# Kernel tuning notes

Measured on AMD Instinct MI355X. Metric: run time of the kernel, lower is better.

## Reference

```python
import jax, jax.numpy as jnp
import numpy as np

V = 32000   # vocab_size
E = 200     # embedding_size
H = 256     # LSTM hidden size (hard-coded in module)
B = 16      # batch
T = 256     # seq_len


def setup_inputs() -> dict:
    key = jax.random.key(0)
    ks = jax.random.split(key, 12)

    def init(k, shape, scale):
        return jax.random.normal(k, shape, jnp.float32) * scale

    inp = {"x": jax.random.randint(ks[0], (B, T), 0, V)}
    inp["emb"] = init(ks[1], (V, E), 0.02)
    dims = [E, H, H]
    s = 1.0 / float(np.sqrt(H))
    for l in range(3):
        inp[f"Wi{l}"] = init(ks[2 + 3 * l], (4 * H, dims[l]), s)  # input weights (gate order i,f,g,o)
        inp[f"Wh{l}"] = init(ks[3 + 3 * l], (4 * H, H), s)        # recurrent weights
        inp[f"b{l}"] = jnp.zeros((4 * H,), jnp.float32)
    inp["fcW"] = init(ks[11], (V, H), s)
    inp["fcb"] = jnp.zeros((V,), jnp.float32)
    return inp


def _lstm_layer(x, Wi, Wh, b):
    # x: [B, T, C_in] -> [B, T, H]; standard LSTM, zero initial state.
    xg = jnp.einsum('btc,gc->btg', x, Wi) + b  # precompute input projections [B,T,4H]
    Hh = Wh.shape[1]

    def step(carry, xt):
        h, c = carry
        g = xt + h @ Wh.T                      # [B, 4H]
        i, f, gg, o = jnp.split(g, 4, axis=-1)
        i = jax.nn.sigmoid(i)
        f = jax.nn.sigmoid(f)
        gg = jnp.tanh(gg)
        o = jax.nn.sigmoid(o)
        c = f * c + i * gg
        h = o * jnp.tanh(c)
        return (h, c), h

    h0 = jnp.zeros((x.shape[0], Hh), x.dtype)
    _, hs = jax.lax.scan(step, (h0, h0), jnp.swapaxes(xg, 0, 1))  # time-major scan
    return jnp.swapaxes(hs, 0, 1)


def reference(x, emb, Wi0, Wh0, b0, Wi1, Wh1, b1, Wi2, Wh2, b2, fcW, fcb):
    out = emb[x]  # [B, T, E]
    for Wi, Wh, b in ((Wi0, Wh0, b0), (Wi1, Wh1, b1), (Wi2, Wh2, b2)):
        out = _lstm_layer(out, Wi, Wh, b)
    logits = out @ fcW.T + fcb  # [B, T, V]
    return jax.nn.log_softmax(logits, axis=-1)
```

## Files before the change

kernel.cpp:

```cpp
#include <hip/hip_runtime.h>
#include <stdint.h>

typedef __attribute__((ext_vector_type(8))) short bf16x8;
typedef __attribute__((ext_vector_type(4))) float f32x4;

#define DEV __device__ __forceinline__

DEV unsigned short f2bf(float f) {
    unsigned b = __float_as_uint(f);
    unsigned r = (b + 0x7fffu + ((b >> 16) & 1u)) >> 16;
    return (unsigned short)r;
}
DEV unsigned pack2(float a, float b) {
    return (unsigned)f2bf(a) | ((unsigned)f2bf(b) << 16);
}
DEV bf16x8 pack8(float4 f0, float4 f1) {
    bf16x8 r;
    r[0] = (short)f2bf(f0.x); r[1] = (short)f2bf(f0.y);
    r[2] = (short)f2bf(f0.z); r[3] = (short)f2bf(f0.w);
    r[4] = (short)f2bf(f1.x); r[5] = (short)f2bf(f1.y);
    r[6] = (short)f2bf(f1.z); r[7] = (short)f2bf(f1.w);
    return r;
}
DEV float sigm(float x) { return 1.f / (1.f + __expf(-x)); }
DEV float tanh_f(float x) {
    float t = __expf(-2.f * fabsf(x));
    float r = (1.f - t) / (1.f + t);
    return copysignf(r, x);
}

#define OFF_HB0   65536
#define OFF_HB1   (65536 + 4194304)
#define OFF_XEA   (65536 + 8388608)
#define OFF_HS    (OFF_XEA + 2097152)

__global__ __launch_bounds__(256) void k_embed(const int* __restrict__ x,
                                               const float* __restrict__ emb,
                                               unsigned short* __restrict__ XeA)
{
    int row = blockIdx.x * 8 + (threadIdx.x >> 5);
    int i = threadIdx.x & 31;
    int tok = x[row];
    int b = row >> 8, t = row & 255;
    uint4 v = make_uint4(0, 0, 0, 0);
    if (i < 25) {
        const float* p = emb + (size_t)tok * 200 + i * 8;
        float4 f0 = *(const float4*)p;
        float4 f1 = *(const float4*)(p + 4);
        v.x = pack2(f0.x, f0.y); v.y = pack2(f0.z, f0.w);
        v.z = pack2(f1.x, f1.y); v.w = pack2(f1.z, f1.w);
    }
    int kt = i >> 2, qq = i & 3;
    *(uint4*)(XeA + (size_t)t * 4096 + (size_t)((kt * 64 + qq * 16 + b) * 8)) = v;
}

template <int OUT_F32>
__global__ __launch_bounds__(256) void k_gemm(const unsigned short* __restrict__ X, int ldx,
                                              const float* __restrict__ W, int K,
                                              const float* __restrict__ bias,
                                              unsigned short* __restrict__ outb,
                                              float* __restrict__ outf, int N)
{
    __shared__ __align__(16) unsigned short Al[128 * 72];
    __shared__ __align__(16) unsigned short Bl[128 * 72];
    const int tid = threadIdx.x, lane = tid & 63, wave = tid >> 6;
    const int wm = wave >> 1, wn = wave & 1;
    const int bm = blockIdx.y, bn = blockIdx.x;
    const int l15 = lane & 15, q = lane >> 4;

    f32x4 acc[4][4];
#pragma unroll
    for (int a = 0; a < 4; a++)
#pragma unroll
        for (int b = 0; b < 4; b++) acc[a][b] = f32x4{0.f, 0.f, 0.f, 0.f};

    for (int kb = 0; kb < 256; kb += 64) {
        __syncthreads();
#pragma unroll
        for (int it = 0; it < 4; ++it) {
            int p = tid + it * 256;
            int row = p >> 3, c8 = p & 7;
            int col = kb + c8 * 8;
            uint4 av = *(const uint4*)(X + (size_t)(bm * 128 + row) * ldx + col);
            *(uint4*)(Al + row * 72 + c8 * 8) = av;
            uint4 bv = make_uint4(0, 0, 0, 0);
            if (col < K) {
                const float* wp = W + (size_t)(bn * 128 + row) * K + col;
                float4 f0 = *(const float4*)wp;
                float4 f1 = *(const float4*)(wp + 4);
                bv.x = pack2(f0.x, f0.y); bv.y = pack2(f0.z, f0.w);
                bv.z = pack2(f1.x, f1.y); bv.w = pack2(f1.z, f1.w);
            }
            *(uint4*)(Bl + row * 72 + c8 * 8) = bv;
        }
        __syncthreads();
#pragma unroll
        for (int kt = 0; kt < 2; ++kt) {
            bf16x8 a[4], b[4];
#pragma unroll
            for (int mt = 0; mt < 4; ++mt)
                a[mt] = *(const bf16x8*)(Al + (wm * 64 + mt * 16 + l15) * 72 + kt * 32 + q * 8);
#pragma unroll
            for (int nt = 0; nt < 4; ++nt)
                b[nt] = *(const bf16x8*)(Bl + (wn * 64 + nt * 16 + l15) * 72 + kt * 32 + q * 8);
#pragma unroll
            for (int mt = 0; mt < 4; ++mt)
#pragma unroll
                for (int nt = 0; nt < 4; ++nt)
                    acc[mt][nt] = __builtin_amdgcn_mfma_f32_16x16x32_bf16(a[mt], b[nt], acc[mt][nt], 0, 0, 0);
        }
    }
#pragma unroll
    for (int nt = 0; nt < 4; ++nt) {
        int gn = bn * 128 + wn * 64 + nt * 16 + l15;
        float bv = bias[gn];
#pragma unroll
        for (int mt = 0; mt < 4; ++mt) {
#pragma unroll
            for (int r = 0; r < 4; ++r) {
                int gm = bm * 128 + wm * 64 + mt * 16 + q * 4 + r;
                float v = acc[mt][nt][r] + bv;
                if (OUT_F32) outf[(size_t)gm * N + gn] = v;
                else outb[(size_t)gm * N + gn] = f2bf(v);
            }
        }
    }
}

__global__ __launch_bounds__(256) void k_scan3(
    const float* __restrict__ Wi0, const float* __restrict__ Wh0, const float* __restrict__ b0,
    const float* __restrict__ Wi1, const float* __restrict__ Wh1, const float* __restrict__ b1,
    const float* __restrict__ Wi2, const float* __restrict__ Wh2, const float* __restrict__ b2,
    const unsigned short* __restrict__ XeA,
    unsigned short* __restrict__ hseq,
    unsigned long long* __restrict__ Hb0,
    unsigned long long* __restrict__ Hb1,
    unsigned long long* __restrict__ ring2)
{
    __shared__ __align__(16) unsigned short hX[4096];
    __shared__ __align__(16) unsigned short hH[4096];
    __shared__ float gbuf[64 * 17];
    const int tid = threadIdx.x, lane = tid & 63, wave = tid >> 6;
    const int L = blockIdx.x >> 4, s = blockIdx.x & 15;
    const int l15 = lane & 15, q = lane >> 4;
    const int grow = wave * 256 + s * 16 + l15;

    const float* Wi = (L == 0) ? Wi0 : ((L == 1) ? Wi1 : Wi2);
    const float* Wh = (L == 0) ? Wh0 : ((L == 1) ? Wh1 : Wh2);
    const float* bb = (L == 0) ? b0 : ((L == 1) ? b1 : b2);
    const int KX = (L == 0) ? 200 : 256;

    bf16x8 WiR[8], WhR[8];
#pragma unroll
    for (int kt = 0; kt < 8; ++kt) {
        int k0 = kt * 32 + q * 8;
        {
            const float* p = Wh + (size_t)grow * 256 + k0;
            WhR[kt] = pack8(*(const float4*)p, *(const float4*)(p + 4));
        }
        if (k0 < KX) {
            const float* p = Wi + (size_t)grow * KX + k0;
            WiR[kt] = pack8(*(const float4*)p, *(const float4*)(p + 4));
        } else {
            WiR[kt] = bf16x8{0, 0, 0, 0, 0, 0, 0, 0};
        }
    }
    const float bv = bb[grow];

    const int eb = tid >> 4, eu = tid & 15;
    const bool pub = (eu & 1) == 0;
    int slot;
    {
        int ug = s * 16 + eu;
        int kt = ug >> 5, qq = (ug >> 3) & 3, j = ug & 7;
        slot = ((kt * 64 + qq * 16 + eb) * 8 + j) >> 1;
    }
    float c = 0.f;
    unsigned* hX32 = (unsigned*)hX;
    unsigned* hH32 = (unsigned*)hH;

    const unsigned long long* xbase = (L == 1) ? Hb0 : Hb1;
    unsigned long long* obase = (L == 0) ? Hb0 : Hb1;
    const unsigned long long* rbase = (L == 0) ? Hb0 : Hb1;

    for (int t = 0; t < 256; ++t) {
        if (L == 0) {
            const unsigned* srcx = (const unsigned*)(XeA + (size_t)t * 4096);
            *(uint4*)(hX32 + tid * 8)     = *(const uint4*)(srcx + tid * 8);
            *(uint4*)(hX32 + tid * 8 + 4) = *(const uint4*)(srcx + tid * 8 + 4);
        }
        {
            unsigned long long vx[8], vh[8];
            unsigned pendx = (L > 0) ? 0xffu : 0u;
            unsigned pendh = (t > 0) ? 0xffu : 0u;
            const unsigned long long* sx = xbase + (size_t)t * 2048 + tid;
            const unsigned long long* sh =
                (L == 2) ? (ring2 + ((t - 1) & 1) * 2048 + tid)
                         : (rbase + (size_t)((t > 0) ? (t - 1) : 0) * 2048 + tid);
            const unsigned ex = (unsigned)(t + 1), eh = (unsigned)t;
            while (pendx | pendh) {
#pragma unroll
                for (int i = 0; i < 8; ++i)
                    if (pendx & (1u << i))
                        vx[i] = __hip_atomic_load(sx + i * 256, __ATOMIC_RELAXED,
                                                  __HIP_MEMORY_SCOPE_AGENT);
#pragma unroll
                for (int i = 0; i < 8; ++i)
                    if (pendh & (1u << i))
                        vh[i] = __hip_atomic_load(sh + i * 256, __ATOMIC_RELAXED,
                                                  __HIP_MEMORY_SCOPE_AGENT);
#pragma unroll
                for (int i = 0; i < 8; ++i) {
                    if ((pendx & (1u << i)) && (unsigned)(vx[i] >> 32) == ex) pendx &= ~(1u << i);
                    if ((pendh & (1u << i)) && (unsigned)(vh[i] >> 32) == eh) pendh &= ~(1u << i);
                }
                if (pendx | pendh) __builtin_amdgcn_s_sleep(1);
            }
            if (L > 0) {
#pragma unroll
                for (int i = 0; i < 8; ++i) hX32[tid + i * 256] = (unsigned)vx[i];
            }
            if (t > 0) {
#pragma unroll
                for (int i = 0; i < 8; ++i) hH32[tid + i * 256] = (unsigned)vh[i];
            } else {
#pragma unroll
                for (int i = 0; i < 8; ++i) hH32[tid + i * 256] = 0u;
            }
        }
        __syncthreads();

        f32x4 acc0 = {bv, bv, bv, bv};
        f32x4 acc1 = {0.f, 0.f, 0.f, 0.f};
#pragma unroll
        for (int kt = 0; kt < 8; ++kt) {
            bf16x8 ax = *(const bf16x8*)(hX + (kt * 64 + lane) * 8);
            acc0 = __builtin_amdgcn_mfma_f32_16x16x32_bf16(ax, WiR[kt], acc0, 0, 0, 0);
            bf16x8 ah = *(const bf16x8*)(hH + (kt * 64 + lane) * 8);
            acc1 = __builtin_amdgcn_mfma_f32_16x16x32_bf16(ah, WhR[kt], acc1, 0, 0, 0);
        }
        {
            int rowb = wave * 16 + l15;
#pragma unroll
            for (int r = 0; r < 4; ++r) gbuf[rowb * 17 + q * 4 + r] = acc0[r] + acc1[r];
        }
        __syncthreads();

        float gi = gbuf[(0 * 16 + eu) * 17 + eb];
        float gf = gbuf[(1 * 16 + eu) * 17 + eb];
        float gg = gbuf[(2 * 16 + eu) * 17 + eb];
        float go = gbuf[(3 * 16 + eu) * 17 + eb];
        float i_ = sigm(gi), f_ = sigm(gf), g_ = tanh_f(gg), o_ = sigm(go);
        c = f_ * c + i_ * g_;
        float h = o_ * tanh_f(c);
        float hn = __shfl_xor(h, 1);
        if (pub) {
            unsigned pk = pack2(h, hn);
            unsigned long long val =
                ((unsigned long long)(unsigned)(t + 1) << 32) | (unsigned long long)pk;
            if (L == 2) {
                __hip_atomic_store(ring2 + (t & 1) * 2048 + slot, val, __ATOMIC_RELAXED,
                                   __HIP_MEMORY_SCOPE_AGENT);
                *(unsigned*)(hseq + (size_t)(eb * 256 + t) * 256 + s * 16 + eu) = pk;
            } else {
                __hip_atomic_store(obase + (size_t)t * 2048 + slot, val, __ATOMIC_RELAXED,
                                   __HIP_MEMORY_SCOPE_AGENT);
            }
        }
    }
}

__global__ __launch_bounds__(1024) void k_lsesub(float* __restrict__ lg)
{
    __shared__ float sm[16], ss[16];
    __shared__ float sL;
    const int row = blockIdx.x, tid = threadIdx.x;
    float* p = lg + (size_t)row * 32000;
    float4 v0[4], v1[4];
    float m = -3.0e38f, s = 0.f;
#pragma unroll
    for (int k = 0; k < 4; ++k) {
        int g = tid + (k << 10);
        if (g < 4000) {
            v0[k] = *(const float4*)(p + g * 8);
            v1[k] = *(const float4*)(p + g * 8 + 4);
            float a0 = fmaxf(fmaxf(v0[k].x, v0[k].y), fmaxf(v0[k].z, v0[k].w));
            float a1 = fmaxf(fmaxf(v1[k].x, v1[k].y), fmaxf(v1[k].z, v1[k].w));
            float ml = fmaxf(a0, a1);
            if (ml > m) { s *= __expf(m - ml); m = ml; }
            s += __expf(v0[k].x - m) + __expf(v0[k].y - m) + __expf(v0[k].z - m) + __expf(v0[k].w - m)
               + __expf(v1[k].x - m) + __expf(v1[k].y - m) + __expf(v1[k].z - m) + __expf(v1[k].w - m);
        }
    }
#pragma unroll
    for (int off = 32; off; off >>= 1) {
        float m2 = __shfl_xor(m, off);
        float s2 = __shfl_xor(s, off);
        float nm = fmaxf(m, m2);
        s = s * __expf(m - nm) + s2 * __expf(m2 - nm);
        m = nm;
    }
    if ((tid & 63) == 0) { sm[tid >> 6] = m; ss[tid >> 6] = s; }
    __syncthreads();
    if (tid == 0) {
        float M = sm[0], S = ss[0];
        for (int w = 1; w < 16; ++w) {
            float m2 = sm[w], s2 = ss[w];
            float nm = fmaxf(M, m2);
            S = S * __expf(M - nm) + s2 * __expf(m2 - nm);
            M = nm;
        }
        sL = M + __logf(S);
    }
    __syncthreads();
    const float L = sL;
#pragma unroll
    for (int k = 0; k < 4; ++k) {
        int g = tid + (k << 10);
        if (g < 4000) {
            v0[k].x -= L; v0[k].y -= L; v0[k].z -= L; v0[k].w -= L;
            v1[k].x -= L; v1[k].y -= L; v1[k].z -= L; v1[k].w -= L;
            *(float4*)(p + g * 8) = v0[k];
            *(float4*)(p + g * 8 + 4) = v1[k];
        }
    }
}

extern "C" void kernel_launch(void* const* d_in, const int* in_sizes, int n_in,
                              void* d_out, int out_size, void* d_ws, size_t ws_size,
                              hipStream_t stream)
{
    const int* x = (const int*)d_in[0];
    const float* emb = (const float*)d_in[1];
    const float* Wi0 = (const float*)d_in[2];
    const float* Wh0 = (const float*)d_in[3];
    const float* b0  = (const float*)d_in[4];
    const float* Wi1 = (const float*)d_in[5];
    const float* Wh1 = (const float*)d_in[6];
    const float* b1  = (const float*)d_in[7];
    const float* Wi2 = (const float*)d_in[8];
    const float* Wh2 = (const float*)d_in[9];
    const float* b2  = (const float*)d_in[10];
    const float* fcW = (const float*)d_in[11];
    const float* fcb = (const float*)d_in[12];
    float* out = (float*)d_out;

    uint8_t* w = (uint8_t*)d_ws;
    unsigned long long* ring2 = (unsigned long long*)w;
    unsigned long long* Hb0 = (unsigned long long*)(w + OFF_HB0);
    unsigned long long* Hb1 = (unsigned long long*)(w + OFF_HB1);
    unsigned short* XeA = (unsigned short*)(w + OFF_XEA);
    unsigned short* hs  = (unsigned short*)(w + OFF_HS);

    hipMemsetAsync(w, 0, OFF_XEA, stream);

    k_embed<<<512, 256, 0, stream>>>(x, emb, XeA);

    k_scan3<<<48, 256, 0, stream>>>(Wi0, Wh0, b0, Wi1, Wh1, b1, Wi2, Wh2, b2,
                                    XeA, hs, Hb0, Hb1, ring2);

    k_gemm<1><<<dim3(250, 32), 256, 0, stream>>>(hs, 256, fcW, 256, fcb, nullptr, out, 32000);

    k_lsesub<<<4096, 1024, 0, stream>>>(out);
}
```

Measured before the change: 1.536 ms.

## Fuse log-softmax into FC GEMM via two-pass recompute with atomic LSE merge

Replaces the separate logits write plus log-softmax read/modify/write pass with two GEMM passes. The first computes per-tile row max/sum-exp and merges them into a global per-row accumulator with 64-bit CAS; the second recomputes the logits and writes them already normalized. It also pre-converts fcW to bf16 once per call so both passes read half-size weights. This trades an extra GEMM's compute and CAS contention for avoiding a full 524MB read plus rewrite of the output.

New measurement: 2.317 ms. +50.9%, slower.

```diff
diff --git a/kernel.cpp b/kernel.cpp
--- a/kernel.cpp
+++ b/kernel.cpp
@@ -33,6 +33,8 @@
 #define OFF_HB1   (65536 + 4194304)
 #define OFF_XEA   (65536 + 8388608)
 #define OFF_HS    (OFF_XEA + 2097152)
+#define OFF_WB    (OFF_HS + 2097152)
+#define WB_BYTES  (32000u * 256u * 2u)
 
 __global__ __launch_bounds__(256) void k_embed(const int* __restrict__ x,
                                                const float* __restrict__ emb,
@@ -54,15 +56,50 @@
     *(uint4*)(XeA + (size_t)t * 4096 + (size_t)((kt * 64 + qq * 16 + b) * 8)) = v;
 }
 
-template <int OUT_F32>
-__global__ __launch_bounds__(256) void k_gemm(const unsigned short* __restrict__ X, int ldx,
-                                              const float* __restrict__ W, int K,
-                                              const float* __restrict__ bias,
-                                              unsigned short* __restrict__ outb,
-                                              float* __restrict__ outf, int N)
+__global__ __launch_bounds__(256) void k_wcvt(const float* __restrict__ W,
+                                              unsigned short* __restrict__ Wb)
+{
+    size_t i = ((size_t)blockIdx.x * 256 + threadIdx.x) * 8;
+    float4 f0 = *(const float4*)(W + i);
+    float4 f1 = *(const float4*)(W + i + 4);
+    uint4 v;
+    v.x = pack2(f0.x, f0.y); v.y = pack2(f0.z, f0.w);
+    v.z = pack2(f1.x, f1.y); v.w = pack2(f1.z, f1.w);
+    *(uint4*)(Wb + i) = v;
+}
+
+DEV void lse_cas_merge(unsigned long long* p, float m, float s)
+{
+    unsigned long long old = __hip_atomic_load(p, __ATOMIC_RELAXED, __HIP_MEMORY_SCOPE_AGENT);
+    while (true) {
+        unsigned long long assumed = old;
+        float mo = __uint_as_float((unsigned)(assumed & 0xffffffffu));
+        float so = __uint_as_float((unsigned)(assumed >> 32));
+        float nm, ns;
+        if (so == 0.f) { nm = m; ns = s; }
+        else {
+            nm = fmaxf(mo, m);
+            ns = so * __expf(mo - nm) + s * __expf(m - nm);
+        }
+        unsigned long long nv =
+            ((unsigned long long)__float_as_uint(ns) << 32) | (unsigned long long)__float_as_uint(nm);
+        old = atomicCAS(p, assumed, nv);
+        if (old == assumed) break;
+    }
+}
+
+template <int WB, int MODE>
+__global__ __launch_bounds__(256) void k_fc(const unsigned short* __restrict__ X,
+                                            const float* __restrict__ W,
+                                            const unsigned short* __restrict__ Wb,
+                                            const float* __restrict__ bias,
+                                            unsigned long long* __restrict__ lacc,
+                                            const float* __restrict__ lse,
+                                            float* __restrict__ outf)
 {
     __shared__ __align__(16) unsigned short Al[128 * 72];
     __shared__ __align__(16) unsigned short Bl[128 * 72];
+    __shared__ float red[2][64][2][2];
     const int tid = threadIdx.x, lane = tid & 63, wave = tid >> 6;
     const int wm = wave >> 1, wn = wave & 1;
     const int bm = blockIdx.y, bn = blockIdx.x;
@@ -81,11 +118,13 @@
             int p = tid + it * 256;
             int row = p >> 3, c8 = p & 7;
             int col = kb + c8 * 8;
-            uint4 av = *(const uint4*)(X + (size_t)(bm * 128 + row) * ldx + col);
+            uint4 av = *(const uint4*)(X + (size_t)(bm * 128 + row) * 256 + col);
             *(uint4*)(Al + row * 72 + c8 * 8) = av;
-            uint4 bv = make_uint4(0, 0, 0, 0);
-            if (col < K) {
-                const float* wp = W + (size_t)(bn * 128 + row) * K + col;
+            uint4 bv;
+            if (WB) {
+                bv = *(const uint4*)(Wb + (size_t)(bn * 128 + row) * 256 + col);
+            } else {
+                const float* wp = W + (size_t)(bn * 128 + row) * 256 + col;
                 float4 f0 = *(const float4*)wp;
                 float4 f1 = *(const float4*)(wp + 4);
                 bv.x = pack2(f0.x, f0.y); bv.y = pack2(f0.z, f0.w);
@@ -110,21 +149,72 @@
                     acc[mt][nt] = __builtin_amdgcn_mfma_f32_16x16x32_bf16(a[mt], b[nt], acc[mt][nt], 0, 0, 0);
         }
     }
-#pragma unroll
-    for (int nt = 0; nt < 4; ++nt) {
-        int gn = bn * 128 + wn * 64 + nt * 16 + l15;
-        float bv = bias[gn];
+
+    if (MODE == 0) {
+        float bvv[4];
+#pragma unroll
+        for (int nt = 0; nt < 4; ++nt) bvv[nt] = bias[bn * 128 + wn * 64 + nt * 16 + l15];
 #pragma unroll
         for (int mt = 0; mt < 4; ++mt) {
 #pragma unroll
             for (int r = 0; r < 4; ++r) {
-                int gm = bm * 128 + wm * 64 + mt * 16 + q * 4 + r;
-                float v = acc[mt][nt][r] + bv;
-                if (OUT_F32) outf[(size_t)gm * N + gn] = v;
-                else outb[(size_t)gm * N + gn] = f2bf(v);
-            }
-        }
-    }
+                float v0 = acc[mt][0][r] + bvv[0];
+                float v1 = acc[mt][1][r] + bvv[1];
+                float v2 = acc[mt][2][r] + bvv[2];
+                float v3 = acc[mt][3][r] + bvv[3];
+                float m = fmaxf(fmaxf(v0, v1), fmaxf(v2, v3));
+#pragma unroll
+                for (int off = 1; off <= 8; off <<= 1) m = fmaxf(m, __shfl_xor(m, off));
+                float s = __expf(v0 - m) + __expf(v1 - m) + __expf(v2 - m) + __expf(v3 - m);
+#pragma unroll
+                for (int off = 1; off <= 8; off <<= 1) s += __shfl_xor(s, off);
+                if (l15 == 0) {
+                    int rl = mt * 16 + q * 4 + r;
+                    red[wm][rl][wn][0] = m;
+                    red[wm][rl][wn][1] = s;
+                }
+            }
+        }
+        __syncthreads();
+        if (tid < 128) {
+            int wmx = tid >> 6, rl = tid & 63;
+            float m0 = red[wmx][rl][0][0], s0 = red[wmx][rl][0][1];
+            float m1 = red[wmx][rl][1][0], s1 = red[wmx][rl][1][1];
+            float nm = fmaxf(m0, m1);
+            float ns = s0 * __expf(m0 - nm) + s1 * __expf(m1 - nm);
+            lse_cas_merge(lacc + bm * 128 + tid, nm, ns);
+        }
+    } else {
+        float lsv[16];
+#pragma unroll
+        for (int mt = 0; mt < 4; ++mt)
+#pragma unroll
+            for (int r = 0; r < 4; ++r)
+                lsv[mt * 4 + r] = lse[bm * 128 + wm * 64 + mt * 16 + q * 4 + r];
+#pragma unroll
+        for (int nt = 0; nt < 4; ++nt) {
+            int gn = bn * 128 + wn * 64 + nt * 16 + l15;
+            float bv = bias[gn];
+#pragma unroll
+            for (int mt = 0; mt < 4; ++mt) {
+#pragma unroll
+                for (int r = 0; r < 4; ++r) {
+                    int gm = bm * 128 + wm * 64 + mt * 16 + q * 4 + r;
+                    outf[(size_t)gm * 32000 + gn] = acc[mt][nt][r] + bv - lsv[mt * 4 + r];
+                }
+            }
+        }
+    }
+}
+
+__global__ __launch_bounds__(256) void k_lsefin(const unsigned long long* __restrict__ lacc,
+                                                float* __restrict__ lse)
+{
+    int i = blockIdx.x * 256 + threadIdx.x;
+    unsigned long long v = lacc[i];
+    float m = __uint_as_float((unsigned)(v & 0xffffffffu));
+    float s = __uint_as_float((unsigned)(v >> 32));
+    lse[i] = m + __logf(s);
 }
 
 __global__ __launch_bounds__(256) void k_scan3(
@@ -270,62 +360,6 @@
     }
 }
 
-__global__ __launch_bounds__(1024) void k_lsesub(float* __restrict__ lg)
-{
-    __shared__ float sm[16], ss[16];
-    __shared__ float sL;
-    const int row = blockIdx.x, tid = threadIdx.x;
-    float* p = lg + (size_t)row * 32000;
-    float4 v0[4], v1[4];
-    float m = -3.0e38f, s = 0.f;
-#pragma unroll
-    for (int k = 0; k < 4; ++k) {
-        int g = tid + (k << 10);
-        if (g < 4000) {
-            v0[k] = *(const float4*)(p + g * 8);
-            v1[k] = *(const float4*)(p + g * 8 + 4);
-            float a0 = fmaxf(fmaxf(v0[k].x, v0[k].y), fmaxf(v0[k].z, v0[k].w));
-            float a1 = fmaxf(fmaxf(v1[k].x, v1[k].y), fmaxf(v1[k].z, v1[k].w));
-            float ml = fmaxf(a0, a1);
-            if (ml > m) { s *= __expf(m - ml); m = ml; }
-            s += __expf(v0[k].x - m) + __expf(v0[k].y - m) + __expf(v0[k].z - m) + __expf(v0[k].w - m)
-               + __expf(v1[k].x - m) + __expf(v1[k].y - m) + __expf(v1[k].z - m) + __expf(v1[k].w - m);
-        }
-    }
-#pragma unroll
-    for (int off = 32; off; off >>= 1) {
-        float m2 = __shfl_xor(m, off);
-        float s2 = __shfl_xor(s, off);
-        float nm = fmaxf(m, m2);
-        s = s * __expf(m - nm) + s2 * __expf(m2 - nm);
-        m = nm;
-    }
-    if ((tid & 63) == 0) { sm[tid >> 6] = m; ss[tid >> 6] = s; }
-    __syncthreads();
-    if (tid == 0) {
-        float M = sm[0], S = ss[0];
-        for (int w = 1; w < 16; ++w) {
-            float m2 = sm[w], s2 = ss[w];
-            float nm = fmaxf(M, m2);
-            S = S * __expf(M - nm) + s2 * __expf(m2 - nm);
-            M = nm;
-        }
-        sL = M + __logf(S);
-    }
-    __syncthreads();
-    const float L = sL;
-#pragma unroll
-    for (int k = 0; k < 4; ++k) {
-        int g = tid + (k << 10);
-        if (g < 4000) {
-            v0[k].x -= L; v0[k].y -= L; v0[k].z -= L; v0[k].w -= L;
-            v1[k].x -= L; v1[k].y -= L; v1[k].z -= L; v1[k].w -= L;
-            *(float4*)(p + g * 8) = v0[k];
-            *(float4*)(p + g * 8 + 4) = v1[k];
-        }
-    }
-}
-
 extern "C" void kernel_launch(void* const* d_in, const int* in_sizes, int n_in,
                               void* d_out, int out_size, void* d_ws, size_t ws_size,
                               hipStream_t stream)
@@ -347,19 +381,31 @@
 
     uint8_t* w = (uint8_t*)d_ws;
     unsigned long long* ring2 = (unsigned long long*)w;
+    unsigned long long* lacc  = (unsigned long long*)(w + 32768);
+    float* lse = (float*)w;
     unsigned long long* Hb0 = (unsigned long long*)(w + OFF_HB0);
     unsigned long long* Hb1 = (unsigned long long*)(w + OFF_HB1);
     unsigned short* XeA = (unsigned short*)(w + OFF_XEA);
     unsigned short* hs  = (unsigned short*)(w + OFF_HS);
+    unsigned short* Wb  = (unsigned short*)(w + OFF_WB);
+    const bool wb_ok = ws_size >= (size_t)OFF_WB + (size_t)WB_BYTES;
 
     hipMemsetAsync(w, 0, OFF_XEA, stream);
+
+    if (wb_ok) k_wcvt<<<4000, 256, 0, stream>>>(fcW, Wb);
 
     k_embed<<<512, 256, 0, stream>>>(x, emb, XeA);
 
     k_scan3<<<48, 256, 0, stream>>>(Wi0, Wh0, b0, Wi1, Wh1, b1, Wi2, Wh2, b2,
                                     XeA, hs, Hb0, Hb1, ring2);
 
-    k_gemm<1><<<dim3(250, 32), 256, 0, stream>>>(hs, 256, fcW, 256, fcb, nullptr, out, 32000);
-
-    k_lsesub<<<4096, 1024, 0, stream>>>(out);
-}
+    if (wb_ok) {
+        k_fc<1, 0><<<dim3(250, 32), 256, 0, stream>>>(hs, nullptr, Wb, fcb, lacc, nullptr, nullptr);
+        k_lsefin<<<16, 256, 0, stream>>>(lacc, lse);
+        k_fc<1, 1><<<dim3(250, 32), 256, 0, stream>>>(hs, nullptr, Wb, fcb, nullptr, lse, out);
+    } else {
+        k_fc<0, 0><<<dim3(250, 32), 256, 0, stream>>>(hs, fcW, nullptr, fcb, lacc, nullptr, nullptr);
+        k_lsefin<<<16, 256, 0, stream>>>(lacc, lse);
+        k_fc<0, 1><<<dim3(250, 32), 256, 0, stream>>>(hs, fcW, nullptr, fcb, nullptr, lse, out);
+    }
+}
```

## Keep FC weight tile resident in LDS across M subtiles and pre-convert weights to bf16

Applied to the files above, without the earlier changes.

The output projection GEMM now loads the full 128x256 bf16 weight tile into swizzled LDS once per block and loops over eight 128-row activation subtiles. Previously every 128x128 output tile re-read and re-converted its fp32 weights. A separate pre-pass converts fcW to bf16 in workspace when enough space exists, which halves the weight bytes read by the GEMM. The cost is 128KB of LDS per block, which allows only one block per CU, plus a grid of just 1000 blocks with serialized subtiles and no load/compute overlap.

After: 1.448 ms. -5.7%, faster.

```diff
diff --git a/kernel.cpp b/kernel.cpp
--- a/kernel.cpp
+++ b/kernel.cpp
@@ -28,11 +28,14 @@
     float r = (1.f - t) / (1.f + t);
     return copysignf(r, x);
 }
+DEV int ldsw(int row, int cb) { return row * 512 + (cb ^ ((row & 7) << 4)); }
 
 #define OFF_HB0   65536
 #define OFF_HB1   (65536 + 4194304)
 #define OFF_XEA   (65536 + 8388608)
 #define OFF_HS    (OFF_XEA + 2097152)
+#define OFF_WB    (OFF_HS + 2097152)
+#define WB_BYTES  (32000u * 256u * 2u)
 
 __global__ __launch_bounds__(256) void k_embed(const int* __restrict__ x,
                                                const float* __restrict__ emb,
@@ -54,75 +57,153 @@
     *(uint4*)(XeA + (size_t)t * 4096 + (size_t)((kt * 64 + qq * 16 + b) * 8)) = v;
 }
 
-template <int OUT_F32>
-__global__ __launch_bounds__(256) void k_gemm(const unsigned short* __restrict__ X, int ldx,
-                                              const float* __restrict__ W, int K,
-                                              const float* __restrict__ bias,
-                                              unsigned short* __restrict__ outb,
-                                              float* __restrict__ outf, int N)
-{
-    __shared__ __align__(16) unsigned short Al[128 * 72];
-    __shared__ __align__(16) unsigned short Bl[128 * 72];
+__global__ __launch_bounds__(256) void k_wcvt(const float* __restrict__ W,
+                                              unsigned short* __restrict__ Wb)
+{
+    size_t i = ((size_t)blockIdx.x * 256 + threadIdx.x) * 8;
+    float4 f0 = *(const float4*)(W + i);
+    float4 f1 = *(const float4*)(W + i + 4);
+    uint4 v;
+    v.x = pack2(f0.x, f0.y); v.y = pack2(f0.z, f0.w);
+    v.z = pack2(f1.x, f1.y); v.w = pack2(f1.z, f1.w);
+    *(uint4*)(Wb + i) = v;
+}
+
+template <int WB>
+__global__ __launch_bounds__(256) void k_fcbig(const unsigned short* __restrict__ X,
+                                               const float* __restrict__ W,
+                                               const unsigned short* __restrict__ Wb,
+                                               const float* __restrict__ bias,
+                                               float* __restrict__ outf)
+{
+    __shared__ __align__(16) char Abuf[65536];
+    __shared__ __align__(16) char Bbuf[65536];
     const int tid = threadIdx.x, lane = tid & 63, wave = tid >> 6;
     const int wm = wave >> 1, wn = wave & 1;
-    const int bm = blockIdx.y, bn = blockIdx.x;
+    const int bn = blockIdx.x, bm = blockIdx.y;
     const int l15 = lane & 15, q = lane >> 4;
 
-    f32x4 acc[4][4];
-#pragma unroll
-    for (int a = 0; a < 4; a++)
-#pragma unroll
-        for (int b = 0; b < 4; b++) acc[a][b] = f32x4{0.f, 0.f, 0.f, 0.f};
-
-    for (int kb = 0; kb < 256; kb += 64) {
+#pragma unroll
+    for (int it = 0; it < 16; ++it) {
+        int p = tid + it * 256;
+        int row = p >> 5, c8 = p & 31;
+        uint4 bv;
+        if (WB) {
+            bv = *(const uint4*)(Wb + (size_t)(bn * 128 + row) * 256 + c8 * 8);
+        } else {
+            const float* wp = W + (size_t)(bn * 128 + row) * 256 + c8 * 8;
+            float4 f0 = *(const float4*)wp;
+            float4 f1 = *(const float4*)(wp + 4);
+            bv.x = pack2(f0.x, f0.y); bv.y = pack2(f0.z, f0.w);
+            bv.z = pack2(f1.x, f1.y); bv.w = pack2(f1.z, f1.w);
+        }
+        *(uint4*)(Bbuf + ldsw(row, c8 * 16)) = bv;
+    }
+
+    float bvv[4];
+#pragma unroll
+    for (int nt = 0; nt < 4; ++nt) bvv[nt] = bias[bn * 128 + wn * 64 + nt * 16 + l15];
+
+    for (int ms = 0; ms < 8; ++ms) {
         __syncthreads();
 #pragma unroll
-        for (int it = 0; it < 4; ++it) {
+        for (int it = 0; it < 16; ++it) {
             int p = tid + it * 256;
-            int row = p >> 3, c8 = p & 7;
-            int col = kb + c8 * 8;
-            uint4 av = *(const uint4*)(X + (size_t)(bm * 128 + row) * ldx + col);
-            *(uint4*)(Al + row * 72 + c8 * 8) = av;
-            uint4 bv = make_uint4(0, 0, 0, 0);
-            if (col < K) {
-                const float* wp = W + (size_t)(bn * 128 + row) * K + col;
-                float4 f0 = *(const float4*)wp;
-                float4 f1 = *(const float4*)(wp + 4);
-                bv.x = pack2(f0.x, f0.y); bv.y = pack2(f0.z, f0.w);
-                bv.z = pack2(f1.x, f1.y); bv.w = pack2(f1.z, f1.w);
-            }
-            *(uint4*)(Bl + row * 72 + c8 * 8) = bv;
+            int row = p >> 5, c8 = p & 31;
+            uint4 av = *(const uint4*)(X + (size_t)(bm * 1024 + ms * 128 + row) * 256 + c8 * 8);
+            *(uint4*)(Abuf + ldsw(row, c8 * 16)) = av;
         }
         __syncthreads();
-#pragma unroll
-        for (int kt = 0; kt < 2; ++kt) {
+
+        f32x4 acc[4][4];
+#pragma unroll
+        for (int a = 0; a < 4; a++)
+#pragma unroll
+            for (int b = 0; b < 4; b++) acc[a][b] = f32x4{0.f, 0.f, 0.f, 0.f};
+
+#pragma unroll
+        for (int kt = 0; kt < 8; ++kt) {
             bf16x8 a[4], b[4];
 #pragma unroll
             for (int mt = 0; mt < 4; ++mt)
-                a[mt] = *(const bf16x8*)(Al + (wm * 64 + mt * 16 + l15) * 72 + kt * 32 + q * 8);
+                a[mt] = *(const bf16x8*)(Abuf + ldsw(wm * 64 + mt * 16 + l15, kt * 64 + q * 16));
 #pragma unroll
             for (int nt = 0; nt < 4; ++nt)
-                b[nt] = *(const bf16x8*)(Bl + (wn * 64 + nt * 16 + l15) * 72 + kt * 32 + q * 8);
+                b[nt] = *(const bf16x8*)(Bbuf + ldsw(wn * 64 + nt * 16 + l15, kt * 64 + q * 16));
 #pragma unroll
             for (int mt = 0; mt < 4; ++mt)
 #pragma unroll
                 for (int nt = 0; nt < 4; ++nt)
                     acc[mt][nt] = __builtin_amdgcn_mfma_f32_16x16x32_bf16(a[mt], b[nt], acc[mt][nt], 0, 0, 0);
         }
-    }
-#pragma unroll
-    for (int nt = 0; nt < 4; ++nt) {
-        int gn = bn * 128 + wn * 64 + nt * 16 + l15;
-        float bv = bias[gn];
-#pragma unroll
-        for (int mt = 0; mt < 4; ++mt) {
-#pragma unroll
-            for (int r = 0; r < 4; ++r) {
-                int gm = bm * 128 + wm * 64 + mt * 16 + q * 4 + r;
-                float v = acc[mt][nt][r] + bv;
-                if (OUT_F32) outf[(size_t)gm * N + gn] = v;
-                else outb[(size_t)gm * N + gn] = f2bf(v);
-            }
+
+#pragma unroll
+        for (int nt = 0; nt < 4; ++nt) {
+            int gn = bn * 128 + wn * 64 + nt * 16 + l15;
+#pragma unroll
+            for (int mt = 0; mt < 4; ++mt) {
+#pragma unroll
+                for (int r = 0; r < 4; ++r) {
+                    int gm = bm * 1024 + ms * 128 + wm * 64 + mt * 16 + q * 4 + r;
+                    outf[(size_t)gm * 32000 + gn] = acc[mt][nt][r] + bvv[nt];
+                }
+            }
+        }
+    }
+}
+
+__global__ __launch_bounds__(1024) void k_lsesub(float* __restrict__ lg)
+{
+    __shared__ float sm[16], ss[16];
+    __shared__ float sL;
+    const int row = blockIdx.x, tid = threadIdx.x;
+    float* p = lg + (size_t)row * 32000;
+    float4 v0[4], v1[4];
+    float m = -3.0e38f, s = 0.f;
+#pragma unroll
+    for (int k = 0; k < 4; ++k) {
+        int g = tid + (k << 10);
+        if (g < 4000) {
+            v0[k] = *(const float4*)(p + g * 8);
+            v1[k] = *(const float4*)(p + g * 8 + 4);
+            float a0 = fmaxf(fmaxf(v0[k].x, v0[k].y), fmaxf(v0[k].z, v0[k].w));
+            float a1 = fmaxf(fmaxf(v1[k].x, v1[k].y), fmaxf(v1[k].z, v1[k].w));
+            float ml = fmaxf(a0, a1);
+            if (ml > m) { s *= __expf(m - ml); m = ml; }
+            s += __expf(v0[k].x - m) + __expf(v0[k].y - m) + __expf(v0[k].z - m) + __expf(v0[k].w - m)
+               + __expf(v1[k].x - m) + __expf(v1[k].y - m) + __expf(v1[k].z - m) + __expf(v1[k].w - m);
+        }
+    }
+#pragma unroll
+    for (int off = 32; off; off >>= 1) {
+        float m2 = __shfl_xor(m, off);
+        float s2 = __shfl_xor(s, off);
+        float nm = fmaxf(m, m2);
+        s = s * __expf(m - nm) + s2 * __expf(m2 - nm);
+        m = nm;
+    }
+    if ((tid & 63) == 0) { sm[tid >> 6] = m; ss[tid >> 6] = s; }
+    __syncthreads();
+    if (tid == 0) {
+        float M = sm[0], S = ss[0];
+        for (int w = 1; w < 16; ++w) {
+            float m2 = sm[w], s2 = ss[w];
+            float nm = fmaxf(M, m2);
+            S = S * __expf(M - nm) + s2 * __expf(m2 - nm);
+            M = nm;
+        }
+        sL = M + __logf(S);
+    }
+    __syncthreads();
+    const float L = sL;
+#pragma unroll
+    for (int k = 0; k < 4; ++k) {
+        int g = tid + (k << 10);
+        if (g < 4000) {
+            v0[k].x -= L; v0[k].y -= L; v0[k].z -= L; v0[k].w -= L;
+            v1[k].x -= L; v1[k].y -= L; v1[k].z -= L; v1[k].w -= L;
+            *(float4*)(p + g * 8) = v0[k];
+            *(float4*)(p + g * 8 + 4) = v1[k];
         }
     }
 }
@@ -270,62 +351,6 @@
     }
 }
 
-__global__ __launch_bounds__(1024) void k_lsesub(float* __restrict__ lg)
-{
-    __shared__ float sm[16], ss[16];
-    __shared__ float sL;
-    const int row = blockIdx.x, tid = threadIdx.x;
-    float* p = lg + (size_t)row * 32000;
-    float4 v0[4], v1[4];
-    float m = -3.0e38f, s = 0.f;
-#pragma unroll
-    for (int k = 0; k < 4; ++k) {
-        int g = tid + (k << 10);
-        if (g < 4000) {
-            v0[k] = *(const float4*)(p + g * 8);
-            v1[k] = *(const float4*)(p + g * 8 + 4);
-            float a0 = fmaxf(fmaxf(v0[k].x, v0[k].y), fmaxf(v0[k].z, v0[k].w));
-            float a1 = fmaxf(fmaxf(v1[k].x, v1[k].y), fmaxf(v1[k].z, v1[k].w));
-            float ml = fmaxf(a0, a1);
-            if (ml > m) { s *= __expf(m - ml); m = ml; }
-            s += __expf(v0[k].x - m) + __expf(v0[k].y - m) + __expf(v0[k].z - m) + __expf(v0[k].w - m)
-               + __expf(v1[k].x - m) + __expf(v1[k].y - m) + __expf(v1[k].z - m) + __expf(v1[k].w - m);
-        }
-    }
-#pragma unroll
-    for (int off = 32; off; off >>= 1) {
-        float m2 = __shfl_xor(m, off);
-        float s2 = __shfl_xor(s, off);
-        float nm = fmaxf(m, m2);
-        s = s * __expf(m - nm) + s2 * __expf(m2 - nm);
-        m = nm;
-    }
-    if ((tid & 63) == 0) { sm[tid >> 6] = m; ss[tid >> 6] = s; }
-    __syncthreads();
-    if (tid == 0) {
-        float M = sm[0], S = ss[0];
-        for (int w = 1; w < 16; ++w) {
-            float m2 = sm[w], s2 = ss[w];
-            float nm = fmaxf(M, m2);
-            S = S * __expf(M - nm) + s2 * __expf(m2 - nm);
-            M = nm;
-        }
-        sL = M + __logf(S);
-    }
-    __syncthreads();
-    const float L = sL;
-#pragma unroll
-    for (int k = 0; k < 4; ++k) {
-        int g = tid + (k << 10);
-        if (g < 4000) {
-            v0[k].x -= L; v0[k].y -= L; v0[k].z -= L; v0[k].w -= L;
-            v1[k].x -= L; v1[k].y -= L; v1[k].z -= L; v1[k].w -= L;
-            *(float4*)(p + g * 8) = v0[k];
-            *(float4*)(p + g * 8 + 4) = v1[k];
-        }
-    }
-}
-
 extern "C" void kernel_launch(void* const* d_in, const int* in_sizes, int n_in,
                               void* d_out, int out_size, void* d_ws, size_t ws_size,
                               hipStream_t stream)
@@ -351,15 +376,22 @@
     unsigned long long* Hb1 = (unsigned long long*)(w + OFF_HB1);
     unsigned short* XeA = (unsigned short*)(w + OFF_XEA);
     unsigned short* hs  = (unsigned short*)(w + OFF_HS);
+    unsigned short* Wb  = (unsigned short*)(w + OFF_WB);
+    const bool wb_ok = ws_size >= (size_t)OFF_WB + (size_t)WB_BYTES;
 
     hipMemsetAsync(w, 0, OFF_XEA, stream);
+
+    if (wb_ok) k_wcvt<<<4000, 256, 0, stream>>>(fcW, Wb);
 
     k_embed<<<512, 256, 0, stream>>>(x, emb, XeA);
 
     k_scan3<<<48, 256, 0, stream>>>(Wi0, Wh0, b0, Wi1, Wh1, b1, Wi2, Wh2, b2,
                                     XeA, hs, Hb0, Hb1, ring2);
 
-    k_gemm<1><<<dim3(250, 32), 256, 0, stream>>>(hs, 256, fcW, 256, fcb, nullptr, out, 32000);
+    if (wb_ok)
+        k_fcbig<1><<<dim3(250, 4), 256, 0, stream>>>(hs, nullptr, Wb, fcb, out);
+    else
+        k_fcbig<0><<<dim3(250, 4), 256, 0, stream>>>(hs, fcW, nullptr, fcb, out);
 
     k_lsesub<<<4096, 1024, 0, stream>>>(out);
 }
```
